# Optimization experiments

Measured on AMD Instinct MI355X. Metric: run time of the kernel, lower is better.

Reference implementation:

```python
import math
import jax, jax.numpy as jnp
import numpy as np

GROUPS = 32
EPS = 1e-5


def group_norm(x, gamma, beta):
    # x: (b, c, h, w); normalize per-group over (c/g, h, w)
    b, c, h, w = x.shape
    xg = x.reshape(b, GROUPS, c // GROUPS, h, w)
    mu = xg.mean(axis=(2, 3, 4), keepdims=True)
    var = xg.var(axis=(2, 3, 4), keepdims=True)
    xn = ((xg - mu) * jax.lax.rsqrt(var + EPS)).reshape(b, c, h, w)
    return xn * gamma[None, :, None, None] + beta[None, :, None, None]


def conv1x1(x, w, bias):
    # x: (b, c, h, w), w: (o, c) -> (b, o, h, w)
    return jnp.einsum('bchw,oc->bohw', x, w) + bias[None, :, None, None]


def setup_inputs() -> dict:
    key = jax.random.key(0)
    ks = jax.random.split(key, 7)
    b, c, h, w = 8, 512, 32, 32
    s = 1.0 / math.sqrt(c)
    return {
        'x': jax.random.normal(ks[0], (b, c, h, w), dtype=jnp.float32),
        'gn_w': jnp.ones((c,), dtype=jnp.float32),
        'gn_b': jnp.zeros((c,), dtype=jnp.float32),
        'qkv_w': jax.random.normal(ks[1], (3 * c, c), dtype=jnp.float32) * s,
        'qkv_b': jnp.zeros((3 * c,), dtype=jnp.float32),
        'proj_w': jax.random.normal(ks[2], (c, c), dtype=jnp.float32) * s,
        'proj_b': jnp.zeros((c,), dtype=jnp.float32),
        'num_heads': 8,
    }


def reference(x, gn_w, gn_b, qkv_w, qkv_b, proj_w, proj_b, num_heads):
    b, c, h, w = x.shape
    hds = num_heads
    d = c // hds
    x_ = group_norm(x, gn_w, gn_b)
    qkv = conv1x1(x_, qkv_w, qkv_b)  # (b, 3c, h, w)
    q, k, v = jnp.split(qkv, 3, axis=1)
    # (b, hds, d, hw)
    q = q.reshape(b, hds, d, h * w)
    k = k.reshape(b, hds, d, h * w)
    v = v.reshape(b, hds, d, h * w)
    # scores: (b, hds, hw, hw) = q^T k / sqrt(d)
    scores = jnp.einsum('bhdq,bhdk->bhqk', q, k) / math.sqrt(d)
    attn = jax.nn.softmax(scores, axis=-1)
    # out = (attn @ v^T)^T -> (b, hds, d, hw)
    out = jnp.einsum('bhqk,bhdk->bhdq', attn, v)
    out = out.reshape(b, c, h, w)
    return x + conv1x1(out, proj_w, proj_b)
```

## Files before the change

### kernel.cpp

```cpp
#include <hip/hip_runtime.h>


typedef __attribute__((ext_vector_type(8))) short short8v;
typedef __attribute__((ext_vector_type(4))) short short4v;
typedef __attribute__((ext_vector_type(4))) float f32x4;
typedef __attribute__((ext_vector_type(2))) unsigned uint2v;

constexpr int Bn = 8, Cn = 512, HWn = 1024, CGn = 16;

#if __has_builtin(__builtin_amdgcn_exp2f)
#define EXP2F(x) __builtin_amdgcn_exp2f(x)
#else
#define EXP2F(x) __exp2f(x)
#endif

static __device__ __forceinline__ short bf16_of(float f) {
  union { float f; unsigned u; } v{f};
  unsigned r = v.u + 0x7fffu + ((v.u >> 16) & 1u);
  return (short)(r >> 16);
}
static __device__ __forceinline__ unsigned bf16pk(float a, float b) {
  return (unsigned)(unsigned short)bf16_of(a) |
         ((unsigned)(unsigned short)bf16_of(b) << 16);
}

static __device__ __forceinline__ void gload16(const void* g, void* l) {
  __builtin_amdgcn_global_load_lds(
      (const __attribute__((address_space(1))) unsigned*)g,
      (__attribute__((address_space(3))) unsigned*)l, 16, 0, 0);
}

__global__ __launch_bounds__(256) void prep_k(const float* __restrict__ x,
                                              float* __restrict__ stats,
                                              const float* __restrict__ wq,
                                              const float* __restrict__ wp,
                                              short* __restrict__ oq,
                                              short* __restrict__ op) {
  if (blockIdx.x >= 256) {
    int i = (blockIdx.x - 256) * 256 + threadIdx.x;
    const float* src = wq;
    short* dst = oq;
    int idx = i;
    if (i >= 196608) { src = wp; dst = op; idx = i - 196608; }
    f32x4 v = ((const f32x4*)src)[idx];
    short4v o;
    o.x = bf16_of(v.x); o.y = bf16_of(v.y); o.z = bf16_of(v.z); o.w = bf16_of(v.w);
    *(short4v*)&dst[idx * 4] = o;
    return;
  }
  int bg = blockIdx.x;
  const f32x4* p = (const f32x4*)(x + (size_t)bg * (CGn * HWn));
  float s = 0.f, ss = 0.f;
  for (int i = threadIdx.x; i < CGn * HWn / 4; i += 256) {
    f32x4 v = p[i];
    s += v.x + v.y + v.z + v.w;
    ss += v.x * v.x + v.y * v.y + v.z * v.z + v.w * v.w;
  }
#pragma unroll
  for (int off = 32; off; off >>= 1) {
    s += __shfl_xor(s, off);
    ss += __shfl_xor(ss, off);
  }
  __shared__ float rs[4], rss[4];
  int lane = threadIdx.x & 63, w = threadIdx.x >> 6;
  if (lane == 0) { rs[w] = s; rss[w] = ss; }
  __syncthreads();
  if (threadIdx.x == 0) {
    float S = rs[0] + rs[1] + rs[2] + rs[3];
    float SS = rss[0] + rss[1] + rss[2] + rss[3];
    const float invn = 1.0f / (CGn * HWn);
    float mu = S * invn;
    float var = SS * invn - mu * mu;
    stats[bg] = mu;
    stats[256 + bg] = rsqrtf(var + 1e-5f);
  }
}

__global__ __launch_bounds__(256) void gn_apply_t_k(const float* __restrict__ x,
                                                    const float* __restrict__ stats,
                                                    const float* __restrict__ gw,
                                                    const float* __restrict__ gb,
                                                    short* __restrict__ xnT) {
  __shared__ __align__(16) short T[64][72];
  const int hw0 = blockIdx.x * 64, c0 = blockIdx.y * 64, b = blockIdx.z;
  const float* xb = x + ((size_t)b * Cn + c0) * HWn + hw0;
  const int t = threadIdx.x;
  const int cr = t >> 4, h4 = (t & 15) * 4;
#pragma unroll
  for (int i = 0; i < 4; i++) {
    int c = cr + 16 * i;
    int cg = c0 + c;
    int bg = b * 32 + (cg >> 4);
    float mu = stats[bg], rstd = stats[256 + bg];
    float ga = gw[cg] * rstd;
    float be = gb[cg] - mu * ga;
    f32x4 v = *(const f32x4*)&xb[(size_t)c * HWn + h4];
    T[h4 + 0][c] = bf16_of(fmaf(v.x, ga, be));
    T[h4 + 1][c] = bf16_of(fmaf(v.y, ga, be));
    T[h4 + 2][c] = bf16_of(fmaf(v.z, ga, be));
    T[h4 + 3][c] = bf16_of(fmaf(v.w, ga, be));
  }
  __syncthreads();
  short* dst = xnT + ((size_t)b * HWn + hw0) * Cn + c0;
  const int hr = t >> 3, c8 = (t & 7) * 8;
#pragma unroll
  for (int i = 0; i < 2; i++) {
    int r = hr + 32 * i;
    *(short8v*)&dst[(size_t)r * Cn + c8] = *(const short8v*)&T[r][c8];
  }
}

__device__ __forceinline__ short8v frag64(const short* buf, int row, int gk) {
  return *(const short8v*)&buf[row * 64 + ((gk ^ (row & 7)) << 3)];
}
__device__ __forceinline__ short8v frag128(const short* buf, int row, int gk) {
  return *(const short8v*)&buf[row * 128 + ((gk ^ (row & 7)) << 3)];
}

template <int MODE>
__global__ __launch_bounds__(256, 2) void gemm_bf16_k(
    const short* __restrict__ A, const short* __restrict__ Bt,
    const float* __restrict__ bias, const float* __restrict__ resid,
    float* __restrict__ outF, short* __restrict__ oQ, short* __restrict__ oK,
    short* __restrict__ oV) {
  constexpr int MB = (MODE == 0) ? 12 : 4;
  const int bid = blockIdx.x;
  const int swz = (bid & 7) * (8 * MB) + (bid >> 3);
  const int bn = swz & 7;
  const int rest = swz >> 3;
  const int bm = rest % MB, b = rest / MB;
  const bool VBLK = (MODE == 0) && (bm >= 8);

  const short* Bb = Bt + (size_t)b * HWn * Cn;
  __shared__ __align__(16) short As[128 * 64];
  __shared__ __align__(16) short Bs[128 * 64];
  const int t = threadIdx.x, l = t & 63, w = t >> 6;
  const int wr = w >> 1, wc = w & 1;
  const int m0 = bm * 128, n0 = bn * 128;
  const f32x4 vzero = {0.f, 0.f, 0.f, 0.f};
  f32x4 acc[4][4];
#pragma unroll
  for (int i = 0; i < 4; i++)
#pragma unroll
    for (int j = 0; j < 4; j++) acc[i][j] = vzero;

  const int sr0 = t >> 3;
  const int sg = t & 7;

  for (int k0 = 0; k0 < 512; k0 += 64) {
#pragma unroll
    for (int it = 0; it < 4; it++) {
      int r = it * 32 + sr0;
      int gs = sg ^ (r & 7);
      gload16(&A[(size_t)(m0 + r) * 512 + k0 + gs * 8], &As[it * 2048 + w * 512]);
      gload16(&Bb[(size_t)(n0 + r) * 512 + k0 + gs * 8], &Bs[it * 2048 + w * 512]);
    }
    __syncthreads();
#pragma unroll
    for (int kk = 0; kk < 2; kk++) {
      short8v af[4], bf[4];
#pragma unroll
      for (int i = 0; i < 4; i++)
        af[i] = frag64(As, wr * 64 + i * 16 + (l & 15), kk * 4 + (l >> 4));
#pragma unroll
      for (int j = 0; j < 4; j++)
        bf[j] = frag64(Bs, wc * 64 + j * 16 + (l & 15), kk * 4 + (l >> 4));
      if (VBLK) {
#pragma unroll
        for (int i = 0; i < 4; i++)
#pragma unroll
          for (int j = 0; j < 4; j++)
            acc[i][j] = __builtin_amdgcn_mfma_f32_16x16x32_bf16(bf[j], af[i], acc[i][j], 0, 0, 0);
      } else {
#pragma unroll
        for (int i = 0; i < 4; i++)
#pragma unroll
          for (int j = 0; j < 4; j++)
            acc[i][j] = __builtin_amdgcn_mfma_f32_16x16x32_bf16(af[i], bf[j], acc[i][j], 0, 0, 0);
      }
    }
    __syncthreads();
  }

  if (MODE == 1) {
    float* outb = outF + (size_t)b * Cn * HWn;
    const float* rb = resid + (size_t)b * Cn * HWn;
#pragma unroll
    for (int i = 0; i < 4; i++) {
      f32x4 bv = *(const f32x4*)&bias[m0 + wr * 64 + i * 16 + (l >> 4) * 4];
#pragma unroll
      for (int r = 0; r < 4; r++) {
        int m = m0 + wr * 64 + i * 16 + (l >> 4) * 4 + r;
#pragma unroll
        for (int j = 0; j < 4; j++) {
          int n = n0 + wc * 64 + j * 16 + (l & 15);
          size_t idx = (size_t)m * HWn + n;
          outb[idx] = acc[i][j][r] + bv[r] + rb[idx];
        }
      }
    }
  } else if (!VBLK) {
    short* oBase = (m0 < 512) ? oQ : oK;
    const int mc = (m0 < 512 ? m0 : m0 - 512) + wr * 64;
#pragma unroll
    for (int i = 0; i < 4; i++) {
      int mi = mc + i * 16 + (l >> 4) * 4;
      f32x4 bv = *(const f32x4*)&bias[m0 + wr * 64 + i * 16 + (l >> 4) * 4];
#pragma unroll
      for (int j = 0; j < 4; j++) {
        int n = n0 + wc * 64 + j * 16 + (l & 15);
        uint2v pk = {bf16pk(acc[i][j][0] + bv[0], acc[i][j][1] + bv[1]),
                     bf16pk(acc[i][j][2] + bv[2], acc[i][j][3] + bv[3])};
        *(uint2v*)&oBase[((size_t)b * HWn + n) * 512 + mi] = pk;
      }
    }
  } else {
#pragma unroll
    for (int i = 0; i < 4; i++) {
      int m = m0 + wr * 64 + i * 16 + (l & 15);
      float bv = bias[m];
      short* vrow = oV + ((size_t)b * 512 + (m - 1024)) * HWn;
#pragma unroll
      for (int j = 0; j < 4; j++) {
        int n = n0 + wc * 64 + j * 16 + (l >> 4) * 4;
        uint2v pk = {bf16pk(acc[i][j][0] + bv, acc[i][j][1] + bv),
                     bf16pk(acc[i][j][2] + bv, acc[i][j][3] + bv)};
        *(uint2v*)&vrow[n] = pk;
      }
    }
  }
}

__global__ __launch_bounds__(512, 4) void attn_k(const short* __restrict__ qT,
                                                 const short* __restrict__ kT,
                                                 const short* __restrict__ vB,
                                                 short* __restrict__ aoT) {
  const int bid = blockIdx.x;
  const int swz = (bid & 7) * 64 + (bid >> 3);
  const int qt = swz & 7, head = (swz >> 3) & 7, b = swz >> 6;
  __shared__ __align__(16) short SM[33792];
  short* Ks = SM;
  short* Vs = SM + 8192;
  short* Ps = SM + 16384;
  const int t = threadIdx.x, l = t & 63, w = t >> 6;
  short* Psw = Ps + w * 2176;
  const f32x4 vzero = {0.f, 0.f, 0.f, 0.f};

  const short* ksrc = kT + (size_t)b * HWn * 512 + head * 64;
  const short* vsrc = vB + ((size_t)b * 512 + head * 64) * HWn;

  const short* qrow = qT +
      ((size_t)b * HWn + qt * 128 + 16 * w + (l & 15)) * 512 + head * 64 +
      (l >> 4) * 8;
  const short8v qf0 = *(const short8v*)&qrow[0];
  const short8v qf1 = *(const short8v*)&qrow[32];

  const int kkv0 = w * 8 + (l >> 3), kg = l & 7;
  const int vd0 = w * 4 + (l >> 4), vg = l & 15;

#pragma unroll
  for (int it = 0; it < 2; it++) {
    int kv = kkv0 + it * 64;
    gload16(&ksrc[(size_t)kv * 512 + (kg ^ (kv & 7)) * 8], &Ks[it * 4096 + w * 512]);
    int d = vd0 + it * 32;
    gload16(&vsrc[(size_t)d * HWn + (vg ^ (d & 7)) * 8], &Vs[it * 4096 + w * 512]);
  }
  __syncthreads();

  f32x4 oa[4];
#pragma unroll
  for (int f = 0; f < 4; f++) oa[f] = vzero;
  float m_run = -1e30f, l_run = 0.f;
  constexpr float SC = 0.1803368801111f;
  constexpr float THRraw = 44.3614195558f;

#pragma unroll 1
  for (int kt = 0; kt < 8; kt++) {
    short8v kreg[2], vreg[2];
    if (kt < 7) {
      const int kt1 = kt + 1;
#pragma unroll
      for (int it = 0; it < 2; it++) {
        int kv = kkv0 + it * 64;
        kreg[it] = *(const short8v*)&ksrc[(size_t)(kt1 * 128 + kv) * 512 +
                                          (kg ^ (kv & 7)) * 8];
        int d = vd0 + it * 32;
        vreg[it] = *(const short8v*)&vsrc[(size_t)d * HWn + kt1 * 128 +
                                          (vg ^ (d & 7)) * 8];
      }
    }

    f32x4 sa[8];
    __builtin_amdgcn_s_setprio(1);
#pragma unroll
    for (int f = 0; f < 8; f++) {
      short8v ka0 = frag64(Ks, 16 * f + (l & 15), l >> 4);
      short8v ka1 = frag64(Ks, 16 * f + (l & 15), (l >> 4) + 4);
      sa[f] = __builtin_amdgcn_mfma_f32_16x16x32_bf16(ka0, qf0, vzero, 0, 0, 0);
      sa[f] = __builtin_amdgcn_mfma_f32_16x16x32_bf16(ka1, qf1, sa[f], 0, 0, 0);
    }
    __builtin_amdgcn_s_setprio(0);

    float mt = -3e38f;
#pragma unroll
    for (int f = 0; f < 8; f++)
#pragma unroll
      for (int r = 0; r < 4; r++) mt = fmaxf(mt, sa[f][r]);
    mt = fmaxf(mt, __shfl_xor(mt, 16));
    mt = fmaxf(mt, __shfl_xor(mt, 32));
    if (__any(mt > m_run + THRraw)) {
      float mn = fmaxf(m_run, mt);
      float corr = EXP2F((m_run - mn) * SC);
      m_run = mn;
      l_run *= corr;
      float cr[4];
#pragma unroll
      for (int r = 0; r < 4; r++) cr[r] = __shfl(corr, 4 * (l >> 4) + r);
#pragma unroll
      for (int f = 0; f < 4; f++)
#pragma unroll
        for (int r = 0; r < 4; r++) oa[f][r] *= cr[r];
    }
    const float mneg = -m_run * SC;
    float ps = 0.f;
#pragma unroll
    for (int f = 0; f < 8; f++)
#pragma unroll
      for (int r = 0; r < 4; r++) {
        float e = EXP2F(fmaf(sa[f][r], SC, mneg));
        sa[f][r] = e;
        ps += e;
      }
    ps += __shfl_xor(ps, 16);
    ps += __shfl_xor(ps, 32);
    l_run += ps;

#pragma unroll
    for (int f = 0; f < 8; f++) {
      int o = (l & 15) * 136 + 16 * f + 4 * (l >> 4);
      uint2v pk = {bf16pk(sa[f][0], sa[f][1]), bf16pk(sa[f][2], sa[f][3])};
      *(uint2v*)&Psw[o] = pk;
    }
    short8v pa[4];
#pragma unroll
    for (int c = 0; c < 4; c++)
      pa[c] = *(const short8v*)&Psw[(l & 15) * 136 + c * 32 + (l >> 4) * 8];
    __builtin_amdgcn_s_setprio(1);
#pragma unroll
    for (int fd = 0; fd < 4; fd++) {
      int row = 16 * fd + (l & 15);
#pragma unroll
      for (int c = 0; c < 4; c++) {
        short8v vb = frag128(Vs, row, c * 4 + (l >> 4));
        oa[fd] = __builtin_amdgcn_mfma_f32_16x16x32_bf16(pa[c], vb, oa[fd], 0, 0, 0);
      }
    }
    __builtin_amdgcn_s_setprio(0);

    if (kt < 7) {
      __syncthreads();
#pragma unroll
      for (int it = 0; it < 2; it++) {
        *(short8v*)&Ks[it * 4096 + w * 512 + l * 8] = kreg[it];
        *(short8v*)&Vs[it * 4096 + w * 512 + l * 8] = vreg[it];
      }
      __syncthreads();
    }
  }

  const float inv = 1.0f / l_run;
  float iv[4];
#pragma unroll
  for (int r = 0; r < 4; r++) iv[r] = __shfl(inv, 4 * (l >> 4) + r);
#pragma unroll
  for (int r = 0; r < 4; r++)
#pragma unroll
    for (int f = 0; f < 4; f++)
      Psw[(4 * (l >> 4) + r) * 136 + 16 * f + (l & 15)] =
          bf16_of(oa[f][r] * iv[r]);
  __syncthreads();
  short* dst = aoT + ((size_t)b * HWn + qt * 128) * 512 + head * 64;
#pragma unroll
  for (int it = 0; it < 2; it++) {
    int r = (t >> 3) + 64 * it;
    int c8 = (t & 7) * 8;
    *(short8v*)&dst[(size_t)r * 512 + c8] =
        *(const short8v*)&Ps[(r >> 4) * 2176 + (r & 15) * 136 + c8];
  }
}

extern "C" void kernel_launch(void* const* d_in, const int* in_sizes, int n_in,
                              void* d_out, int out_size, void* d_ws, size_t ws_size,
                              hipStream_t stream) {
  const float* x = (const float*)d_in[0];
  const float* gn_w = (const float*)d_in[1];
  const float* gn_b = (const float*)d_in[2];
  const float* qkv_w = (const float*)d_in[3];
  const float* qkv_b = (const float*)d_in[4];
  const float* proj_w = (const float*)d_in[5];
  const float* proj_b = (const float*)d_in[6];
  float* out = (float*)d_out;

  char* ws = (char*)d_ws;
  float* stats = (float*)ws;
  short* wqb = (short*)(ws + 4096);
  short* wpb = (short*)(ws + 4096 + 1572864);
  char* p = ws + 4096 + 1572864 + 524288;
  const size_t SB = (size_t)Bn * HWn * 512 * 2;
  short* xnT = (short*)p;
  short* qT = (short*)(p + SB);
  short* kT = (short*)(p + 2 * SB);
  short* vB = (short*)(p + 3 * SB);
  short* aoT = (short*)(p + 4 * SB);

  prep_k<<<1280, 256, 0, stream>>>(x, stats, qkv_w, proj_w, wqb, wpb);
  gn_apply_t_k<<<dim3(16, 8, 8), 256, 0, stream>>>(x, stats, gn_w, gn_b, xnT);
  gemm_bf16_k<0><<<768, 256, 0, stream>>>(wqb, xnT, qkv_b, nullptr, nullptr, qT, kT, vB);
  attn_k<<<512, 512, 0, stream>>>(qT, kT, vB, aoT);
  gemm_bf16_k<1><<<256, 256, 0, stream>>>(wpb, aoT, proj_b, x, out, nullptr,
                                          nullptr, nullptr);
}
```

Before: 85.32 us.

## Fuse group-norm stats and apply into one pass with blocked layout; widen proj GEMM

Merges the statistics kernel and the normalize/transpose kernel into one kernel that keeps each group's 16 channels in registers and writes a channel-blocked bf16 layout (16-channel groups, hw-major). This removes one launch and a second read of x. The QKV GEMM's B-operand loads are changed to index that blocked layout. The projection GEMM is split into its own kernel with 512 threads per block and a smaller per-wave tile, trading more waves for fewer accumulators per wave.

```diff
diff --git a/kernel.cpp b/kernel.cpp
--- a/kernel.cpp
+++ b/kernel.cpp
@@ -5,8 +5,9 @@
 typedef __attribute__((ext_vector_type(4))) short short4v;
 typedef __attribute__((ext_vector_type(4))) float f32x4;
 typedef __attribute__((ext_vector_type(2))) unsigned uint2v;
-
-constexpr int Bn = 8, Cn = 512, HWn = 1024, CGn = 16;
+typedef __attribute__((ext_vector_type(4))) unsigned uint4v;
+
+constexpr int Bn = 8, Cn = 512, HWn = 1024;
 
 #if __has_builtin(__builtin_amdgcn_exp2f)
 #define EXP2F(x) __builtin_amdgcn_exp2f(x)
@@ -30,14 +31,17 @@
       (__attribute__((address_space(3))) unsigned*)l, 16, 0, 0);
 }
 
-__global__ __launch_bounds__(256) void prep_k(const float* __restrict__ x,
-                                              float* __restrict__ stats,
-                                              const float* __restrict__ wq,
-                                              const float* __restrict__ wp,
-                                              short* __restrict__ oq,
-                                              short* __restrict__ op) {
+__global__ __launch_bounds__(256) void gn_fused_k(const float* __restrict__ x,
+                                                  const float* __restrict__ gw,
+                                                  const float* __restrict__ gb,
+                                                  const float* __restrict__ wq,
+                                                  const float* __restrict__ wp,
+                                                  short* __restrict__ oq,
+                                                  short* __restrict__ op,
+                                                  short* __restrict__ xn3) {
+  const int t = threadIdx.x;
   if (blockIdx.x >= 256) {
-    int i = (blockIdx.x - 256) * 256 + threadIdx.x;
+    int i = (blockIdx.x - 256) * 256 + t;
     const float* src = wq;
     short* dst = oq;
     int idx = i;
@@ -48,13 +52,16 @@
     *(short4v*)&dst[idx * 4] = o;
     return;
   }
-  int bg = blockIdx.x;
-  const f32x4* p = (const f32x4*)(x + (size_t)bg * (CGn * HWn));
+  const int bg = blockIdx.x;
+  const int g = bg & 31;
+  const f32x4* src = (const f32x4*)(x + (size_t)bg * 16384);
+  f32x4 v[16];
   float s = 0.f, ss = 0.f;
-  for (int i = threadIdx.x; i < CGn * HWn / 4; i += 256) {
-    f32x4 v = p[i];
-    s += v.x + v.y + v.z + v.w;
-    ss += v.x * v.x + v.y * v.y + v.z * v.z + v.w * v.w;
+#pragma unroll
+  for (int k = 0; k < 16; k++) {
+    v[k] = src[t + 256 * k];
+    s += v[k].x + v[k].y + v[k].z + v[k].w;
+    ss += v[k].x * v[k].x + v[k].y * v[k].y + v[k].z * v[k].z + v[k].w * v[k].w;
   }
 #pragma unroll
   for (int off = 32; off; off >>= 1) {
@@ -62,51 +69,33 @@
     ss += __shfl_xor(ss, off);
   }
   __shared__ float rs[4], rss[4];
-  int lane = threadIdx.x & 63, w = threadIdx.x >> 6;
+  const int lane = t & 63, w = t >> 6;
   if (lane == 0) { rs[w] = s; rss[w] = ss; }
   __syncthreads();
-  if (threadIdx.x == 0) {
-    float S = rs[0] + rs[1] + rs[2] + rs[3];
-    float SS = rss[0] + rss[1] + rss[2] + rss[3];
-    const float invn = 1.0f / (CGn * HWn);
-    float mu = S * invn;
-    float var = SS * invn - mu * mu;
-    stats[bg] = mu;
-    stats[256 + bg] = rsqrtf(var + 1e-5f);
-  }
-}
-
-__global__ __launch_bounds__(256) void gn_apply_t_k(const float* __restrict__ x,
-                                                    const float* __restrict__ stats,
-                                                    const float* __restrict__ gw,
-                                                    const float* __restrict__ gb,
-                                                    short* __restrict__ xnT) {
-  __shared__ __align__(16) short T[64][72];
-  const int hw0 = blockIdx.x * 64, c0 = blockIdx.y * 64, b = blockIdx.z;
-  const float* xb = x + ((size_t)b * Cn + c0) * HWn + hw0;
-  const int t = threadIdx.x;
-  const int cr = t >> 4, h4 = (t & 15) * 4;
-#pragma unroll
-  for (int i = 0; i < 4; i++) {
-    int c = cr + 16 * i;
-    int cg = c0 + c;
-    int bg = b * 32 + (cg >> 4);
-    float mu = stats[bg], rstd = stats[256 + bg];
-    float ga = gw[cg] * rstd;
-    float be = gb[cg] - mu * ga;
-    f32x4 v = *(const f32x4*)&xb[(size_t)c * HWn + h4];
-    T[h4 + 0][c] = bf16_of(fmaf(v.x, ga, be));
-    T[h4 + 1][c] = bf16_of(fmaf(v.y, ga, be));
-    T[h4 + 2][c] = bf16_of(fmaf(v.z, ga, be));
-    T[h4 + 3][c] = bf16_of(fmaf(v.w, ga, be));
-  }
-  __syncthreads();
-  short* dst = xnT + ((size_t)b * HWn + hw0) * Cn + c0;
-  const int hr = t >> 3, c8 = (t & 7) * 8;
-#pragma unroll
-  for (int i = 0; i < 2; i++) {
-    int r = hr + 32 * i;
-    *(short8v*)&dst[(size_t)r * Cn + c8] = *(const short8v*)&T[r][c8];
+  const float S = rs[0] + rs[1] + rs[2] + rs[3];
+  const float SS = rss[0] + rss[1] + rss[2] + rss[3];
+  constexpr float invn = 1.0f / 16384.f;
+  const float mu = S * invn;
+  const float var = SS * invn - mu * mu;
+  const float rstd = rsqrtf(var + 1e-5f);
+  float ga[16], be[16];
+#pragma unroll
+  for (int k = 0; k < 16; k++) {
+    ga[k] = gw[g * 16 + k] * rstd;
+    be[k] = gb[g * 16 + k] - mu * ga[k];
+  }
+  short* dst = xn3 + (size_t)bg * 16384;
+#pragma unroll
+  for (int d = 0; d < 4; d++) {
+    unsigned pk[8];
+#pragma unroll
+    for (int k = 0; k < 16; k += 2)
+      pk[k >> 1] = bf16pk(fmaf(v[k][d], ga[k], be[k]),
+                          fmaf(v[k + 1][d], ga[k + 1], be[k + 1]));
+    uint4v lo = {pk[0], pk[1], pk[2], pk[3]};
+    uint4v hi = {pk[4], pk[5], pk[6], pk[7]};
+    *(uint4v*)&dst[(4 * t + d) * 16] = lo;
+    *(uint4v*)&dst[(4 * t + d) * 16 + 8] = hi;
   }
 }
 
@@ -117,19 +106,111 @@
   return *(const short8v*)&buf[row * 128 + ((gk ^ (row & 7)) << 3)];
 }
 
-template <int MODE>
-__global__ __launch_bounds__(256, 2) void gemm_bf16_k(
+__global__ __launch_bounds__(256, 2) void gemm_qkv_k(
+    const short* __restrict__ A, const short* __restrict__ xn3,
+    const float* __restrict__ bias, short* __restrict__ oQ,
+    short* __restrict__ oK, short* __restrict__ oV) {
+  const int bid = blockIdx.x;
+  const int swz = (bid & 7) * 96 + (bid >> 3);
+  const int bn = swz & 7;
+  const int rest = swz >> 3;
+  const int bm = rest % 12, b = rest / 12;
+  const bool VBLK = (bm >= 8);
+
+  const short* Bb = xn3 + (size_t)b * 524288;
+  __shared__ __align__(16) short As[128 * 64];
+  __shared__ __align__(16) short Bs[128 * 64];
+  const int t = threadIdx.x, l = t & 63, w = t >> 6;
+  const int wr = w >> 1, wc = w & 1;
+  const int m0 = bm * 128, n0 = bn * 128;
+  const f32x4 vzero = {0.f, 0.f, 0.f, 0.f};
+  f32x4 acc[4][4];
+#pragma unroll
+  for (int i = 0; i < 4; i++)
+#pragma unroll
+    for (int j = 0; j < 4; j++) acc[i][j] = vzero;
+
+  const int sr0 = t >> 3;
+  const int sg = t & 7;
+
+  for (int k0 = 0; k0 < 512; k0 += 64) {
+#pragma unroll
+    for (int it = 0; it < 4; it++) {
+      int r = it * 32 + sr0;
+      int gs = sg ^ (r & 7);
+      gload16(&A[(size_t)(m0 + r) * 512 + k0 + gs * 8], &As[it * 2048 + w * 512]);
+      int gp = (k0 >> 4) + (gs >> 1);
+      gload16(&Bb[(size_t)((gp << 10) + n0 + r) * 16 + ((gs & 1) << 3)],
+              &Bs[it * 2048 + w * 512]);
+    }
+    __syncthreads();
+#pragma unroll
+    for (int kk = 0; kk < 2; kk++) {
+      short8v af[4], bf[4];
+#pragma unroll
+      for (int i = 0; i < 4; i++)
+        af[i] = frag64(As, wr * 64 + i * 16 + (l & 15), kk * 4 + (l >> 4));
+#pragma unroll
+      for (int j = 0; j < 4; j++)
+        bf[j] = frag64(Bs, wc * 64 + j * 16 + (l & 15), kk * 4 + (l >> 4));
+      if (VBLK) {
+#pragma unroll
+        for (int i = 0; i < 4; i++)
+#pragma unroll
+          for (int j = 0; j < 4; j++)
+            acc[i][j] = __builtin_amdgcn_mfma_f32_16x16x32_bf16(bf[j], af[i], acc[i][j], 0, 0, 0);
+      } else {
+#pragma unroll
+        for (int i = 0; i < 4; i++)
+#pragma unroll
+          for (int j = 0; j < 4; j++)
+            acc[i][j] = __builtin_amdgcn_mfma_f32_16x16x32_bf16(af[i], bf[j], acc[i][j], 0, 0, 0);
+      }
+    }
+    __syncthreads();
+  }
+
+  if (!VBLK) {
+    short* oBase = (m0 < 512) ? oQ : oK;
+    const int mc = (m0 < 512 ? m0 : m0 - 512) + wr * 64;
+#pragma unroll
+    for (int i = 0; i < 4; i++) {
+      int mi = mc + i * 16 + (l >> 4) * 4;
+      f32x4 bv = *(const f32x4*)&bias[m0 + wr * 64 + i * 16 + (l >> 4) * 4];
+#pragma unroll
+      for (int j = 0; j < 4; j++) {
+        int n = n0 + wc * 64 + j * 16 + (l & 15);
+        uint2v pk = {bf16pk(acc[i][j][0] + bv[0], acc[i][j][1] + bv[1]),
+                     bf16pk(acc[i][j][2] + bv[2], acc[i][j][3] + bv[3])};
+        *(uint2v*)&oBase[((size_t)b * HWn + n) * 512 + mi] = pk;
+      }
+    }
+  } else {
+#pragma unroll
+    for (int i = 0; i < 4; i++) {
+      int m = m0 + wr * 64 + i * 16 + (l & 15);
+      float bv = bias[m];
+      short* vrow = oV + ((size_t)b * 512 + (m - 1024)) * HWn;
+#pragma unroll
+      for (int j = 0; j < 4; j++) {
+        int n = n0 + wc * 64 + j * 16 + (l >> 4) * 4;
+        uint2v pk = {bf16pk(acc[i][j][0] + bv, acc[i][j][1] + bv),
+                     bf16pk(acc[i][j][2] + bv, acc[i][j][3] + bv)};
+        *(uint2v*)&vrow[n] = pk;
+      }
+    }
+  }
+}
+
+__global__ __launch_bounds__(512, 2) void gemm_proj_k(
     const short* __restrict__ A, const short* __restrict__ Bt,
     const float* __restrict__ bias, const float* __restrict__ resid,
-    float* __restrict__ outF, short* __restrict__ oQ, short* __restrict__ oK,
-    short* __restrict__ oV) {
-  constexpr int MB = (MODE == 0) ? 12 : 4;
+    float* __restrict__ outF) {
   const int bid = blockIdx.x;
-  const int swz = (bid & 7) * (8 * MB) + (bid >> 3);
+  const int swz = (bid & 7) * 32 + (bid >> 3);
   const int bn = swz & 7;
   const int rest = swz >> 3;
-  const int bm = rest % MB, b = rest / MB;
-  const bool VBLK = (MODE == 0) && (bm >= 8);
+  const int bm = rest & 3, b = rest >> 2;
 
   const short* Bb = Bt + (size_t)b * HWn * Cn;
   __shared__ __align__(16) short As[128 * 64];
@@ -138,9 +219,9 @@
   const int wr = w >> 1, wc = w & 1;
   const int m0 = bm * 128, n0 = bn * 128;
   const f32x4 vzero = {0.f, 0.f, 0.f, 0.f};
-  f32x4 acc[4][4];
-#pragma unroll
-  for (int i = 0; i < 4; i++)
+  f32x4 acc[2][4];
+#pragma unroll
+  for (int i = 0; i < 2; i++)
 #pragma unroll
     for (int j = 0; j < 4; j++) acc[i][j] = vzero;
 
@@ -149,83 +230,44 @@
 
   for (int k0 = 0; k0 < 512; k0 += 64) {
 #pragma unroll
-    for (int it = 0; it < 4; it++) {
-      int r = it * 32 + sr0;
+    for (int it = 0; it < 2; it++) {
+      int r = it * 64 + sr0;
       int gs = sg ^ (r & 7);
-      gload16(&A[(size_t)(m0 + r) * 512 + k0 + gs * 8], &As[it * 2048 + w * 512]);
-      gload16(&Bb[(size_t)(n0 + r) * 512 + k0 + gs * 8], &Bs[it * 2048 + w * 512]);
+      gload16(&A[(size_t)(m0 + r) * 512 + k0 + gs * 8], &As[it * 4096 + w * 512]);
+      gload16(&Bb[(size_t)(n0 + r) * 512 + k0 + gs * 8], &Bs[it * 4096 + w * 512]);
     }
     __syncthreads();
 #pragma unroll
     for (int kk = 0; kk < 2; kk++) {
-      short8v af[4], bf[4];
-#pragma unroll
-      for (int i = 0; i < 4; i++)
-        af[i] = frag64(As, wr * 64 + i * 16 + (l & 15), kk * 4 + (l >> 4));
+      short8v af[2], bf[4];
+#pragma unroll
+      for (int i = 0; i < 2; i++)
+        af[i] = frag64(As, wr * 32 + i * 16 + (l & 15), kk * 4 + (l >> 4));
 #pragma unroll
       for (int j = 0; j < 4; j++)
         bf[j] = frag64(Bs, wc * 64 + j * 16 + (l & 15), kk * 4 + (l >> 4));
-      if (VBLK) {
-#pragma unroll
-        for (int i = 0; i < 4; i++)
-#pragma unroll
-          for (int j = 0; j < 4; j++)
-            acc[i][j] = __builtin_amdgcn_mfma_f32_16x16x32_bf16(bf[j], af[i], acc[i][j], 0, 0, 0);
-      } else {
-#pragma unroll
-        for (int i = 0; i < 4; i++)
-#pragma unroll
-          for (int j = 0; j < 4; j++)
-            acc[i][j] = __builtin_amdgcn_mfma_f32_16x16x32_bf16(af[i], bf[j], acc[i][j], 0, 0, 0);
-      }
+#pragma unroll
+      for (int i = 0; i < 2; i++)
+#pragma unroll
+        for (int j = 0; j < 4; j++)
+          acc[i][j] = __builtin_amdgcn_mfma_f32_16x16x32_bf16(af[i], bf[j], acc[i][j], 0, 0, 0);
     }
     __syncthreads();
   }
 
-  if (MODE == 1) {
-    float* outb = outF + (size_t)b * Cn * HWn;
-    const float* rb = resid + (size_t)b * Cn * HWn;
-#pragma unroll
-    for (int i = 0; i < 4; i++) {
-      f32x4 bv = *(const f32x4*)&bias[m0 + wr * 64 + i * 16 + (l >> 4) * 4];
-#pragma unroll
-      for (int r = 0; r < 4; r++) {
-        int m = m0 + wr * 64 + i * 16 + (l >> 4) * 4 + r;
-#pragma unroll
-        for (int j = 0; j < 4; j++) {
-          int n = n0 + wc * 64 + j * 16 + (l & 15);
-          size_t idx = (size_t)m * HWn + n;
-          outb[idx] = acc[i][j][r] + bv[r] + rb[idx];
-        }
-      }
-    }
-  } else if (!VBLK) {
-    short* oBase = (m0 < 512) ? oQ : oK;
-    const int mc = (m0 < 512 ? m0 : m0 - 512) + wr * 64;
-#pragma unroll
-    for (int i = 0; i < 4; i++) {
-      int mi = mc + i * 16 + (l >> 4) * 4;
-      f32x4 bv = *(const f32x4*)&bias[m0 + wr * 64 + i * 16 + (l >> 4) * 4];
+  float* outb = outF + (size_t)b * Cn * HWn;
+  const float* rb = resid + (size_t)b * Cn * HWn;
+#pragma unroll
+  for (int i = 0; i < 2; i++) {
+    f32x4 bv = *(const f32x4*)&bias[m0 + wr * 32 + i * 16 + (l >> 4) * 4];
+#pragma unroll
+    for (int r = 0; r < 4; r++) {
+      int m = m0 + wr * 32 + i * 16 + (l >> 4) * 4 + r;
 #pragma unroll
       for (int j = 0; j < 4; j++) {
         int n = n0 + wc * 64 + j * 16 + (l & 15);
-        uint2v pk = {bf16pk(acc[i][j][0] + bv[0], acc[i][j][1] + bv[1]),
-                     bf16pk(acc[i][j][2] + bv[2], acc[i][j][3] + bv[3])};
-        *(uint2v*)&oBase[((size_t)b * HWn + n) * 512 + mi] = pk;
-      }
-    }
-  } else {
-#pragma unroll
-    for (int i = 0; i < 4; i++) {
-      int m = m0 + wr * 64 + i * 16 + (l & 15);
-      float bv = bias[m];
-      short* vrow = oV + ((size_t)b * 512 + (m - 1024)) * HWn;
-#pragma unroll
-      for (int j = 0; j < 4; j++) {
-        int n = n0 + wc * 64 + j * 16 + (l >> 4) * 4;
-        uint2v pk = {bf16pk(acc[i][j][0] + bv, acc[i][j][1] + bv),
-                     bf16pk(acc[i][j][2] + bv, acc[i][j][3] + bv)};
-        *(uint2v*)&vrow[n] = pk;
+        size_t idx = (size_t)m * HWn + n;
+        outb[idx] = acc[i][j][r] + bv[r] + rb[idx];
       }
     }
   }
@@ -402,21 +444,18 @@
   float* out = (float*)d_out;
 
   char* ws = (char*)d_ws;
-  float* stats = (float*)ws;
   short* wqb = (short*)(ws + 4096);
   short* wpb = (short*)(ws + 4096 + 1572864);
   char* p = ws + 4096 + 1572864 + 524288;
   const size_t SB = (size_t)Bn * HWn * 512 * 2;
-  short* xnT = (short*)p;
+  short* xn3 = (short*)p;
   short* qT = (short*)(p + SB);
   short* kT = (short*)(p + 2 * SB);
   short* vB = (short*)(p + 3 * SB);
   short* aoT = (short*)(p + 4 * SB);
 
-  prep_k<<<1280, 256, 0, stream>>>(x, stats, qkv_w, proj_w, wqb, wpb);
-  gn_apply_t_k<<<dim3(16, 8, 8), 256, 0, stream>>>(x, stats, gn_w, gn_b, xnT);
-  gemm_bf16_k<0><<<768, 256, 0, stream>>>(wqb, xnT, qkv_b, nullptr, nullptr, qT, kT, vB);
+  gn_fused_k<<<1280, 256, 0, stream>>>(x, gn_w, gn_b, qkv_w, proj_w, wqb, wpb, xn3);
+  gemm_qkv_k<<<768, 256, 0, stream>>>(wqb, xn3, qkv_b, qT, kT, vB);
   attn_k<<<512, 512, 0, stream>>>(qT, kT, vB, aoT);
-  gemm_bf16_k<1><<<256, 256, 0, stream>>>(wpb, aoT, proj_b, x, out, nullptr,
-                                          nullptr, nullptr);
-}
+  gemm_proj_k<<<256, 512, 0, stream>>>(wpb, aoT, proj_b, x, out);
+}
```

Result: faster. 81.82 us (-4.1%).
